# Kernel optimization log

Measured on AMD Instinct MI355X. Metric: run time of the kernel, lower is better.

Reference implementation:

```python
import jax, jax.numpy as jnp
import numpy as np

NS = 100000   # s-nodes (dtype==1, destinations)
NE = 100000   # e-nodes (dtype==2, sources)
EDG = 1600000 # edges e->s, avg degree 16
D = 256       # in_dim == out_dim
H = 8         # heads
HD = D // H   # head dim 32
FEAT = 64     # dst 'feat' size (hardcoded dstfeat_fc input)
DFF = 512     # ffn inner hidden


def setup_inputs() -> dict:
    key = jax.random.key(0)
    ks = jax.random.split(key, 12)
    s = jax.random.normal(ks[0], (NS, D), jnp.float32)
    e = jax.random.normal(ks[1], (NE, D), jnp.float32)
    dst_feat = jax.random.normal(ks[2], (NS, FEAT), jnp.float32)
    edge_src = jax.random.randint(ks[3], (EDG,), 0, NE)
    # guarantee every s-node has >=1 in-edge (first NS edges hit each dst once)
    rnd_dst = jax.random.randint(ks[4], (EDG,), 0, NS)
    edge_dst = jnp.where(jnp.arange(EDG) < NS, jnp.arange(EDG) % NS, rnd_dst)
    fc_w = jax.random.normal(ks[5], (H, D, HD), jnp.float32) / np.sqrt(D)
    dstfeat_w = jax.random.normal(ks[6], (H, FEAT, HD), jnp.float32) / np.sqrt(FEAT)
    proj_w = jax.random.normal(ks[7], (2 * D, D), jnp.float32) / np.sqrt(2 * D)
    proj_b = jnp.zeros((D,), jnp.float32)
    ln_g = jnp.ones((D,), jnp.float32)
    ln_b = jnp.zeros((D,), jnp.float32)
    w1 = jax.random.normal(ks[8], (D, DFF), jnp.float32) / np.sqrt(D)
    b1 = jnp.zeros((DFF,), jnp.float32)
    w2 = jax.random.normal(ks[9], (DFF, D), jnp.float32) / np.sqrt(DFF)
    b2 = jnp.zeros((D,), jnp.float32)
    return dict(s=s, e=e, dst_feat=dst_feat, fc_w=fc_w, dstfeat_w=dstfeat_w,
                proj_w=proj_w, proj_b=proj_b, ln_g=ln_g, ln_b=ln_b,
                w1=w1, b1=b1, w2=w2, b2=b2,
                edge_src=edge_src, edge_dst=edge_dst)


def _segment_softmax(scores, seg, n):
    # scores: [E, H], seg: [E] dst ids
    smax = jax.ops.segment_max(scores, seg, num_segments=n)  # [n, H], -inf for empty
    smax = jnp.where(jnp.isfinite(smax), smax, 0.0)
    ex = jnp.exp(scores - smax[seg])
    denom = jax.ops.segment_sum(ex, seg, num_segments=n)
    denom = jnp.where(denom > 0, denom, 1.0)
    return ex / denom[seg]


def reference(s, e, dst_feat, fc_w, dstfeat_w, proj_w, proj_b,
              ln_g, ln_b, w1, b1, w2, b2, edge_src, edge_dst):
    # per-head linear on source (e-node) features: [NE, H, HD]
    z = jnp.einsum('ni,hio->nho', e, fc_w)
    # per-head dst feature projection: [NS, H, HD]
    df = jnp.einsum('nf,hfo->nho', dst_feat, dstfeat_w)
    zs = z[edge_src]       # [E, H, HD] gather
    dfe = df[edge_dst]     # [E, H, HD]
    score = jnp.sum(zs * dfe, axis=-1)          # [E, H] per-edge dot score
    alpha = _segment_softmax(score, edge_dst, NS)
    hh = jax.ops.segment_sum(alpha[..., None] * zs, edge_dst, num_segments=NS)  # [NS, H, HD]
    h = hh.reshape(NS, H * HD)                  # concat heads
    h = jax.nn.elu(h)
    h = jnp.concatenate([h, s], axis=-1) @ proj_w + proj_b  # proj(cat(h, origin=s))
    # PositionwiseFeedForward (pre-LN, residual, gelu); dropout off (eval)
    mu = jnp.mean(h, axis=-1, keepdims=True)
    var = jnp.var(h, axis=-1, keepdims=True)
    xn = (h - mu) * jax.lax.rsqrt(var + 1e-6) * ln_g + ln_b
    out = h + (jax.nn.gelu(xn @ w1 + b1) @ w2 + b2)
    return out
```

## Files before the change

### kernel.cpp

```cpp
#include <hip/hip_runtime.h>
#include <hip/hip_bf16.h>
#include <stdint.h>

#define NS_N 100000
#define NE_N 100000
#define MP 100096
#define EDG_N 1600000
#define DIM 256
#define FEAT_N 64
#define DFF_N 512

using bf16 = __hip_bfloat16;
typedef __bf16 bf16x8 __attribute__((ext_vector_type(8)));
typedef float f32x4 __attribute__((ext_vector_type(4)));

__device__ __forceinline__ float toF(float x) { return x; }
__device__ __forceinline__ float toF(bf16 x) { return __bfloat162float(x); }

template <class T> __device__ __forceinline__ T fromF(float x);
template <> __device__ __forceinline__ float fromF<float>(float x) { return x; }
template <> __device__ __forceinline__ bf16 fromF<bf16>(float x) { return __float2bfloat16(x); }

__device__ __forceinline__ void g2l16(const void* g, void* l) {
    __builtin_amdgcn_global_load_lds((const __attribute__((address_space(1))) unsigned int*)g,
                                     (__attribute__((address_space(3))) unsigned int*)l, 16, 0, 0);
}

__global__ void cvt_f2b4(const float4* __restrict__ src, bf16* __restrict__ dst,
                         int M, int K4, int S) {
    int idx = blockIdx.x * 256 + threadIdx.x;
    if (idx >= M * K4) return;
    int r = idx / K4, c = (idx - r * K4) * 4;
    float4 v = src[idx];
    union { ushort4 u; bf16 h[4]; } p;
    p.h[0] = fromF<bf16>(v.x); p.h[1] = fromF<bf16>(v.y);
    p.h[2] = fromF<bf16>(v.z); p.h[3] = fromF<bf16>(v.w);
    *(ushort4*)&dst[(size_t)r * S + c] = p.u;
}

__global__ void tr_w(const float* __restrict__ src, bf16* __restrict__ dst, int K, int N) {
    int idx = blockIdx.x * 256 + threadIdx.x;
    if (idx >= K * N) return;
    int n = idx / K, k = idx - n * K;
    dst[idx] = fromF<bf16>(src[(size_t)k * N + n]);
}

__global__ void tr_headw(const float* __restrict__ src, bf16* __restrict__ dst, int K) {
    int idx = blockIdx.x * 256 + threadIdx.x;
    if (idx >= 256 * K) return;
    int n = idx / K, k = idx - n * K;
    dst[idx] = fromF<bf16>(src[((size_t)(n >> 5) * K + k) * 32 + (n & 31)]);
}

__global__ void count_edges(const int* __restrict__ edst, int* __restrict__ counts) {
    int t = blockIdx.x * 256 + threadIdx.x;
    if (t < EDG_N) atomicAdd(&counts[edst[t]], 1);
}

__global__ void scan_block(const int* __restrict__ counts, int* __restrict__ partial,
                           int* __restrict__ chunk) {
    __shared__ int sh[512];
    int i = blockIdx.x * 512 + threadIdx.x;
    int v = (i < NS_N) ? counts[i] : 0;
    sh[threadIdx.x] = v;
    __syncthreads();
    for (int off = 1; off < 512; off <<= 1) {
        int x = (threadIdx.x >= off) ? sh[threadIdx.x - off] : 0;
        __syncthreads();
        sh[threadIdx.x] += x;
        __syncthreads();
    }
    if (i < NS_N) partial[i] = sh[threadIdx.x] - v;
    if (threadIdx.x == 511) chunk[blockIdx.x] = sh[511];
}

__global__ void scan_chunks(int* __restrict__ chunk, int nc) {
    __shared__ int sh[256];
    int t = threadIdx.x;
    int v = (t < nc) ? chunk[t] : 0;
    sh[t] = v;
    __syncthreads();
    for (int off = 1; off < 256; off <<= 1) {
        int x = (t >= off) ? sh[t - off] : 0;
        __syncthreads();
        sh[t] += x;
        __syncthreads();
    }
    if (t < nc) chunk[t] = sh[t] - v;
}

__global__ void add_offsets(int* __restrict__ rowst, const int* __restrict__ chunk,
                            int* __restrict__ cursor) {
    int i = blockIdx.x * 256 + threadIdx.x;
    if (i < NS_N) {
        int r = rowst[i] + chunk[i >> 9];
        rowst[i] = r;
        cursor[i] = r;
    }
}

__global__ void scatter_edges(const int* __restrict__ esrc, const int* __restrict__ edst,
                              int* __restrict__ cursor, int* __restrict__ csr) {
    int t = blockIdx.x * 256 + threadIdx.x;
    if (t < EDG_N) {
        int d = edst[t];
        int pos = atomicAdd(&cursor[d], 1);
        csr[pos] = esrc[t];
    }
}

template <class TC, bool BIAS, bool GELU, bool RES>
__global__ __launch_bounds__(256) void mfma_gemm(
    const bf16* __restrict__ A, const bf16* __restrict__ BT,
    const float* __restrict__ bias, const float* __restrict__ res,
    TC* __restrict__ C, int M, int N, int K) {
    __shared__ bf16 As[128 * 32];
    __shared__ bf16 Bs[128 * 32];
    const int tid = threadIdx.x;
    const int wave = tid >> 6, lane = tid & 63;
    const int m0 = blockIdx.y * 128, n0 = blockIdx.x * 128;
    const int wm = (wave >> 1) * 64, wn = (wave & 1) * 64;

    f32x4 acc[4][4];
    const f32x4 zero4 = {0.f, 0.f, 0.f, 0.f};
#pragma unroll
    for (int i = 0; i < 4; i++)
#pragma unroll
        for (int j = 0; j < 4; j++) acc[i][j] = zero4;

    const int sr = lane >> 2, sc = (lane & 3) * 8;
    const bf16* gA0 = A + (size_t)(m0 + wave * 16 + sr) * K + sc;
    const bf16* gA1 = A + (size_t)(m0 + 64 + wave * 16 + sr) * K + sc;
    const bf16* gB0 = BT + (size_t)(n0 + wave * 16 + sr) * K + sc;
    const bf16* gB1 = BT + (size_t)(n0 + 64 + wave * 16 + sr) * K + sc;
    bf16* lA0 = As + wave * 512;
    bf16* lA1 = As + (wave + 4) * 512;
    bf16* lB0 = Bs + wave * 512;
    bf16* lB1 = Bs + (wave + 4) * 512;

    const int fr = lane & 15, fq = (lane >> 4) * 8;

    for (int k0 = 0; k0 < K; k0 += 32) {
        __syncthreads();
        g2l16(gA0, lA0);
        g2l16(gA1, lA1);
        g2l16(gB0, lB0);
        g2l16(gB1, lB1);
        gA0 += 32; gA1 += 32; gB0 += 32; gB1 += 32;
        __syncthreads();
        bf16x8 af[4], bfv[4];
#pragma unroll
        for (int mt = 0; mt < 4; mt++)
            af[mt] = *(const bf16x8*)&As[(wm + mt * 16 + fr) * 32 + fq];
#pragma unroll
        for (int nt = 0; nt < 4; nt++)
            bfv[nt] = *(const bf16x8*)&Bs[(wn + nt * 16 + fr) * 32 + fq];
#pragma unroll
        for (int mt = 0; mt < 4; mt++)
#pragma unroll
            for (int nt = 0; nt < 4; nt++)
                acc[mt][nt] = __builtin_amdgcn_mfma_f32_16x16x32_bf16(af[mt], bfv[nt], acc[mt][nt], 0, 0, 0);
    }

    const int q4 = (lane >> 4) * 4;
#pragma unroll
    for (int nt = 0; nt < 4; nt++) {
        const int col = n0 + wn + nt * 16 + fr;
        const float bv = BIAS ? bias[col] : 0.f;
#pragma unroll
        for (int mt = 0; mt < 4; mt++) {
#pragma unroll
            for (int r = 0; r < 4; r++) {
                int row = m0 + wm + mt * 16 + q4 + r;
                if (row < M) {
                    float v = acc[mt][nt][r] + bv;
                    if (GELU) {
                        float x = v;
                        v = 0.5f * x * (1.f + tanhf(0.7978845608028654f * (x + 0.044715f * x * x * x)));
                    }
                    if (RES) v += res[(size_t)row * N + col];
                    C[(size_t)row * N + col] = fromF<TC>(v);
                }
            }
        }
    }
}

__device__ __forceinline__ float4 ldz4(const bf16* __restrict__ p) {
    ushort4 u = *(const ushort4*)p;
    float4 f;
    f.x = toF(*(const bf16*)&u.x);
    f.y = toF(*(const bf16*)&u.y);
    f.z = toF(*(const bf16*)&u.z);
    f.w = toF(*(const bf16*)&u.w);
    return f;
}

__device__ __forceinline__ float dot4(float4 a, float4 b) {
    return fmaf(a.x, b.x, fmaf(a.y, b.y, fmaf(a.z, b.z, a.w * b.w)));
}

__device__ __forceinline__ float hred8(float p) {
    p += __shfl_xor(p, 1);
    p += __shfl_xor(p, 2);
    p += __shfl_xor(p, 4);
    return p;
}

__global__ __launch_bounds__(256) void attn_k(
    const bf16* __restrict__ z, const bf16* __restrict__ df,
    const int* __restrict__ rowst, const int* __restrict__ counts,
    const int* __restrict__ csr, bf16* __restrict__ he) {
    const int dst = blockIdx.x * 4 + (threadIdx.x >> 6);
    if (dst >= NS_N) return;
    const int lane = threadIdx.x & 63;
    const int c4 = lane * 4;

    float4 dfv = ldz4(&df[(size_t)dst * DIM + c4]);

    const int rs = rowst[dst], deg = counts[dst];
    float m = -1e30f, l = 0.f;
    float4 acc = {0.f, 0.f, 0.f, 0.f};

    for (int c0 = 0; c0 < deg; c0 += 64) {
        const int nc = min(64, deg - c0);
        int idx = (lane < nc) ? csr[rs + c0 + lane] : 0;
        int j = 0;
        for (; j + 4 <= nc; j += 4) {
            int s0 = __shfl(idx, j);
            int s1 = __shfl(idx, j + 1);
            int s2 = __shfl(idx, j + 2);
            int s3 = __shfl(idx, j + 3);
            float4 z0 = ldz4(&z[(size_t)s0 * DIM + c4]);
            float4 z1 = ldz4(&z[(size_t)s1 * DIM + c4]);
            float4 z2 = ldz4(&z[(size_t)s2 * DIM + c4]);
            float4 z3 = ldz4(&z[(size_t)s3 * DIM + c4]);
            float p0 = hred8(dot4(z0, dfv));
            float p1 = hred8(dot4(z1, dfv));
            float p2 = hred8(dot4(z2, dfv));
            float p3 = hred8(dot4(z3, dfv));
            float nm = fmaxf(m, fmaxf(fmaxf(p0, p1), fmaxf(p2, p3)));
            float e0 = __expf(m - nm);
            float w0 = __expf(p0 - nm);
            float w1 = __expf(p1 - nm);
            float w2 = __expf(p2 - nm);
            float w3 = __expf(p3 - nm);
            l = fmaf(l, e0, (w0 + w1) + (w2 + w3));
            acc.x = fmaf(acc.x, e0, fmaf(w0, z0.x, fmaf(w1, z1.x, fmaf(w2, z2.x, w3 * z3.x))));
            acc.y = fmaf(acc.y, e0, fmaf(w0, z0.y, fmaf(w1, z1.y, fmaf(w2, z2.y, w3 * z3.y))));
            acc.z = fmaf(acc.z, e0, fmaf(w0, z0.z, fmaf(w1, z1.z, fmaf(w2, z2.z, w3 * z3.z))));
            acc.w = fmaf(acc.w, e0, fmaf(w0, z0.w, fmaf(w1, z1.w, fmaf(w2, z2.w, w3 * z3.w))));
            m = nm;
        }
        for (; j < nc; ++j) {
            int s0 = __shfl(idx, j);
            float4 z0 = ldz4(&z[(size_t)s0 * DIM + c4]);
            float p0 = hred8(dot4(z0, dfv));
            float nm = fmaxf(m, p0);
            float e0 = __expf(m - nm);
            float w0 = __expf(p0 - nm);
            l = fmaf(l, e0, w0);
            acc.x = fmaf(acc.x, e0, w0 * z0.x);
            acc.y = fmaf(acc.y, e0, w0 * z0.y);
            acc.z = fmaf(acc.z, e0, w0 * z0.z);
            acc.w = fmaf(acc.w, e0, w0 * z0.w);
            m = nm;
        }
    }

    const float invl = 1.f / l;
    float hx = acc.x * invl, hy = acc.y * invl, hz = acc.z * invl, hw = acc.w * invl;
    hx = (hx > 0.f) ? hx : expm1f(hx);
    hy = (hy > 0.f) ? hy : expm1f(hy);
    hz = (hz > 0.f) ? hz : expm1f(hz);
    hw = (hw > 0.f) ? hw : expm1f(hw);
    union { ushort4 u; bf16 h[4]; } o;
    o.h[0] = fromF<bf16>(hx);
    o.h[1] = fromF<bf16>(hy);
    o.h[2] = fromF<bf16>(hz);
    o.h[3] = fromF<bf16>(hw);
    *(ushort4*)&he[(size_t)dst * 512 + c4] = o.u;
}

__global__ __launch_bounds__(256) void ln_k(const float* __restrict__ h1,
                                            const float* __restrict__ g,
                                            const float* __restrict__ b,
                                            bf16* __restrict__ xn) {
    int row = blockIdx.x, t = threadIdx.x;
    float x = h1[(size_t)row * DIM + t];
    float s1 = x, s2 = x * x;
#pragma unroll
    for (int off = 32; off > 0; off >>= 1) {
        s1 += __shfl_xor(s1, off, 64);
        s2 += __shfl_xor(s2, off, 64);
    }
    __shared__ float red[2][4];
    int w = t >> 6;
    if ((t & 63) == 0) {
        red[0][w] = s1;
        red[1][w] = s2;
    }
    __syncthreads();
    float t1 = red[0][0] + red[0][1] + red[0][2] + red[0][3];
    float t2 = red[1][0] + red[1][1] + red[1][2] + red[1][3];
    float mu = t1 * (1.f / DIM);
    float var = t2 * (1.f / DIM) - mu * mu;
    float v = (x - mu) * rsqrtf(var + 1e-6f) * g[t] + b[t];
    xn[(size_t)row * DIM + t] = fromF<bf16>(v);
}

extern "C" void kernel_launch(void* const* d_in, const int* in_sizes, int n_in,
                              void* d_out, int out_size, void* d_ws, size_t ws_size,
                              hipStream_t stream) {
    const float* s = (const float*)d_in[0];
    const float* e = (const float*)d_in[1];
    const float* dst_feat = (const float*)d_in[2];
    const float* fc_w = (const float*)d_in[3];
    const float* dstfeat_w = (const float*)d_in[4];
    const float* proj_w = (const float*)d_in[5];
    const float* proj_b = (const float*)d_in[6];
    const float* ln_g = (const float*)d_in[7];
    const float* ln_b = (const float*)d_in[8];
    const float* w1 = (const float*)d_in[9];
    const float* b1 = (const float*)d_in[10];
    const float* w2 = (const float*)d_in[11];
    const float* b2 = (const float*)d_in[12];
    const int* edge_src = (const int*)d_in[13];
    const int* edge_dst = (const int*)d_in[14];
    float* out = (float*)d_out;

    char* base = (char*)d_ws;
    size_t off = 0;
    auto alloc = [&](size_t bytes) -> char* {
        char* p = base + off;
        off = (off + bytes + 255) & ~(size_t)255;
        return p;
    };
    bf16* fcT = (bf16*)alloc((size_t)256 * 256 * 2);
    bf16* dfeatT = (bf16*)alloc((size_t)256 * 64 * 2);
    bf16* projT = (bf16*)alloc((size_t)256 * 512 * 2);
    bf16* w1T = (bf16*)alloc((size_t)512 * 256 * 2);
    bf16* w2T = (bf16*)alloc((size_t)256 * 512 * 2);
    int* counts = (int*)alloc((size_t)NS_N * 4);
    int* rowst = (int*)alloc((size_t)NS_N * 4);
    int* cursor = (int*)alloc((size_t)NS_N * 4);
    int* chunks = (int*)alloc(1024);
    int* csr = (int*)alloc((size_t)EDG_N * 4);
    bf16* eB = (bf16*)alloc((size_t)MP * DIM * 2);
    bf16* zB = (bf16*)alloc((size_t)MP * DIM * 2);
    bf16* dfB = (bf16*)alloc((size_t)MP * DIM * 2);
    bf16* dfeatB = (bf16*)alloc((size_t)MP * FEAT_N * 2);
    bf16* catB = (bf16*)alloc((size_t)MP * 512 * 2);
    float* h1F = (float*)alloc((size_t)MP * DIM * 4);
    bf16* xnB = eB;
    bf16* a1B = zB;

    hipMemsetAsync(counts, 0, (size_t)NS_N * 4, stream);
    tr_headw<<<(256 * 256 + 255) / 256, 256, 0, stream>>>(fc_w, fcT, 256);
    tr_headw<<<(256 * 64 + 255) / 256, 256, 0, stream>>>(dstfeat_w, dfeatT, 64);
    tr_w<<<(512 * 256 + 255) / 256, 256, 0, stream>>>(proj_w, projT, 512, 256);
    tr_w<<<(256 * 512 + 255) / 256, 256, 0, stream>>>(w1, w1T, 256, 512);
    tr_w<<<(512 * 256 + 255) / 256, 256, 0, stream>>>(w2, w2T, 512, 256);
    cvt_f2b4<<<(NE_N * 64 + 255) / 256, 256, 0, stream>>>((const float4*)e, eB, NE_N, 64, DIM);
    cvt_f2b4<<<(NS_N * 16 + 255) / 256, 256, 0, stream>>>((const float4*)dst_feat, dfeatB, NS_N, 16, FEAT_N);
    cvt_f2b4<<<(NS_N * 64 + 255) / 256, 256, 0, stream>>>((const float4*)s, catB + 256, NS_N, 64, 512);
    count_edges<<<(EDG_N + 255) / 256, 256, 0, stream>>>(edge_dst, counts);
    int nchunk = (NS_N + 511) / 512;
    scan_block<<<nchunk, 512, 0, stream>>>(counts, rowst, chunks);
    scan_chunks<<<1, 256, 0, stream>>>(chunks, nchunk);
    add_offsets<<<(NS_N + 255) / 256, 256, 0, stream>>>(rowst, chunks, cursor);
    scatter_edges<<<(EDG_N + 255) / 256, 256, 0, stream>>>(edge_src, edge_dst, cursor, csr);

    dim3 blk(256);
    const int gy = MP / 128;
    mfma_gemm<bf16, false, false, false><<<dim3(2, gy), blk, 0, stream>>>(
        eB, fcT, nullptr, nullptr, zB, NE_N, DIM, DIM);
    mfma_gemm<bf16, false, false, false><<<dim3(2, gy), blk, 0, stream>>>(
        dfeatB, dfeatT, nullptr, nullptr, dfB, NS_N, DIM, FEAT_N);
    attn_k<<<(NS_N + 3) / 4, 256, 0, stream>>>(zB, dfB, rowst, counts, csr, catB);
    mfma_gemm<float, true, false, false><<<dim3(2, gy), blk, 0, stream>>>(
        catB, projT, proj_b, nullptr, h1F, NS_N, DIM, 2 * DIM);
    ln_k<<<NS_N, 256, 0, stream>>>(h1F, ln_g, ln_b, xnB);
    mfma_gemm<bf16, true, true, false><<<dim3(4, gy), blk, 0, stream>>>(
        xnB, w1T, b1, nullptr, a1B, NS_N, DFF_N, DIM);
    mfma_gemm<float, true, false, true><<<dim3(2, gy), blk, 0, stream>>>(
        a1B, w2T, b2, h1F, out, NS_N, DIM, DFF_N);
}
```

Measured before the change: 1.088 ms.

## Triple-buffer GEMM LDS tiles with async prefetch and XOR-swizzled layout

The MFMA GEMM now keeps three LDS buffers and issues global-to-LDS loads two k-tiles ahead. It waits with explicit vmcnt counts instead of a full sync before each tile, so memory latency overlaps the MFMA work. It also XOR-swizzles the column placement of each 16-byte chunk, both when loading global data into LDS and when reading fragments, to cut LDS bank conflicts. LDS use triples, which may lower occupancy. The hand-written waitcnt counts assume a fixed number of outstanding loads per stage.

```diff
diff --git a/kernel.cpp b/kernel.cpp
--- a/kernel.cpp
+++ b/kernel.cpp
@@ -114,8 +114,8 @@
     const bf16* __restrict__ A, const bf16* __restrict__ BT,
     const float* __restrict__ bias, const float* __restrict__ res,
     TC* __restrict__ C, int M, int N, int K) {
-    __shared__ bf16 As[128 * 32];
-    __shared__ bf16 Bs[128 * 32];
+    __shared__ bf16 As[3][128 * 32];
+    __shared__ bf16 Bs[3][128 * 32];
     const int tid = threadIdx.x;
     const int wave = tid >> 6, lane = tid & 63;
     const int m0 = blockIdx.y * 128, n0 = blockIdx.x * 128;
@@ -128,44 +128,60 @@
 #pragma unroll
         for (int j = 0; j < 4; j++) acc[i][j] = zero4;
 
-    const int sr = lane >> 2, sc = (lane & 3) * 8;
-    const bf16* gA0 = A + (size_t)(m0 + wave * 16 + sr) * K + sc;
-    const bf16* gA1 = A + (size_t)(m0 + 64 + wave * 16 + sr) * K + sc;
-    const bf16* gB0 = BT + (size_t)(n0 + wave * 16 + sr) * K + sc;
-    const bf16* gB1 = BT + (size_t)(n0 + 64 + wave * 16 + sr) * K + sc;
-    bf16* lA0 = As + wave * 512;
-    bf16* lA1 = As + (wave + 4) * 512;
-    bf16* lB0 = Bs + wave * 512;
-    bf16* lB1 = Bs + (wave + 4) * 512;
-
-    const int fr = lane & 15, fq = (lane >> 4) * 8;
-
-    for (int k0 = 0; k0 < K; k0 += 32) {
-        __syncthreads();
-        g2l16(gA0, lA0);
-        g2l16(gA1, lA1);
-        g2l16(gB0, lB0);
-        g2l16(gB1, lB1);
-        gA0 += 32; gA1 += 32; gB0 += 32; gB1 += 32;
-        __syncthreads();
+    const int sr = lane >> 2;
+    const int scs = (((lane & 3) ^ ((lane >> 3) & 3)) * 8);
+    const bf16* gA0 = A + (size_t)(m0 + wave * 16 + sr) * K + scs;
+    const bf16* gA1 = A + (size_t)(m0 + 64 + wave * 16 + sr) * K + scs;
+    const bf16* gB0 = BT + (size_t)(n0 + wave * 16 + sr) * K + scs;
+    const bf16* gB1 = BT + (size_t)(n0 + 64 + wave * 16 + sr) * K + scs;
+
+    const int nt = K >> 5;
+
+    auto stage = [&](int kt, int b) {
+        const int ko = kt << 5;
+        g2l16(gA0 + ko, &As[b][wave * 512]);
+        g2l16(gA1 + ko, &As[b][(wave + 4) * 512]);
+        g2l16(gB0 + ko, &Bs[b][wave * 512]);
+        g2l16(gB1 + ko, &Bs[b][(wave + 4) * 512]);
+    };
+
+    stage(0, 0);
+    if (nt > 1) stage(1, 1);
+
+    const int fr = lane & 15;
+    const int pslot = ((((lane >> 4) ^ ((fr >> 1) & 3))) << 4);
+
+    int buf = 0;
+    for (int t = 0; t < nt; ++t) {
+        if (t + 2 < nt) stage(t + 2, buf == 0 ? 2 : buf - 1);
+        if (t + 2 < nt)      asm volatile("s_waitcnt vmcnt(8)" ::: "memory");
+        else if (t + 1 < nt) asm volatile("s_waitcnt vmcnt(4)" ::: "memory");
+        else                 asm volatile("s_waitcnt vmcnt(0)" ::: "memory");
+        __builtin_amdgcn_s_barrier();
+        asm volatile("" ::: "memory");
+        const char* Ab = (const char*)As[buf];
+        const char* Bb = (const char*)Bs[buf];
         bf16x8 af[4], bfv[4];
 #pragma unroll
         for (int mt = 0; mt < 4; mt++)
-            af[mt] = *(const bf16x8*)&As[(wm + mt * 16 + fr) * 32 + fq];
-#pragma unroll
-        for (int nt = 0; nt < 4; nt++)
-            bfv[nt] = *(const bf16x8*)&Bs[(wn + nt * 16 + fr) * 32 + fq];
+            af[mt] = *(const bf16x8*)(Ab + (wm + mt * 16 + fr) * 64 + pslot);
+#pragma unroll
+        for (int jt = 0; jt < 4; jt++)
+            bfv[jt] = *(const bf16x8*)(Bb + (wn + jt * 16 + fr) * 64 + pslot);
 #pragma unroll
         for (int mt = 0; mt < 4; mt++)
 #pragma unroll
-            for (int nt = 0; nt < 4; nt++)
-                acc[mt][nt] = __builtin_amdgcn_mfma_f32_16x16x32_bf16(af[mt], bfv[nt], acc[mt][nt], 0, 0, 0);
+            for (int jt = 0; jt < 4; jt++)
+                acc[mt][jt] = __builtin_amdgcn_mfma_f32_16x16x32_bf16(af[mt], bfv[jt], acc[mt][jt], 0, 0, 0);
+        asm volatile("" ::: "memory");
+        __builtin_amdgcn_s_barrier();
+        buf = (buf == 2) ? 0 : buf + 1;
     }
 
     const int q4 = (lane >> 4) * 4;
 #pragma unroll
-    for (int nt = 0; nt < 4; nt++) {
-        const int col = n0 + wn + nt * 16 + fr;
+    for (int jt = 0; jt < 4; jt++) {
+        const int col = n0 + wn + jt * 16 + fr;
         const float bv = BIAS ? bias[col] : 0.f;
 #pragma unroll
         for (int mt = 0; mt < 4; mt++) {
@@ -173,7 +189,7 @@
             for (int r = 0; r < 4; r++) {
                 int row = m0 + wm + mt * 16 + q4 + r;
                 if (row < M) {
-                    float v = acc[mt][nt][r] + bv;
+                    float v = acc[mt][jt][r] + bv;
                     if (GELU) {
                         float x = v;
                         v = 0.5f * x * (1.f + tanhf(0.7978845608028654f * (x + 0.044715f * x * x * x)));
```

Result: no change. 1.069 ms (-1.7%).

## Rewrite GEMMs as full-K A-stationary tiles with B streamed from global

Applied to the files above, without the earlier changes.

Replaces the 128x128 K-looped GEMM with a kernel that loads a whole 64xK A panel into swizzled LDS once. Each wave then sweeps output column blocks, streaming B fragments directly from global memory (L2-resident weights) with register double buffering. The aim is to drop per-K-step barriers and the redundant A reloads across column blocks. It also folds bias and residual into the accumulator init and swaps tanhf for an exp-based tanh in GELU. LDS use grows to 64 KB for K=512, which may limit occupancy, and global B loads may add latency.

```diff
diff --git a/kernel.cpp b/kernel.cpp
--- a/kernel.cpp
+++ b/kernel.cpp
@@ -109,77 +109,100 @@
     }
 }
 
-template <class TC, bool BIAS, bool GELU, bool RES>
-__global__ __launch_bounds__(256) void mfma_gemm(
+template <int K, int N, class TC, bool BIAS, bool GELU, bool RES>
+__global__ __launch_bounds__(256) void mfma_gemm2(
     const bf16* __restrict__ A, const bf16* __restrict__ BT,
     const float* __restrict__ bias, const float* __restrict__ res,
-    TC* __restrict__ C, int M, int N, int K) {
-    __shared__ bf16 As[128 * 32];
-    __shared__ bf16 Bs[128 * 32];
+    TC* __restrict__ C, int M) {
+    static_assert(K % 32 == 0 && N % 256 == 0, "shape");
+    constexpr int KS = K / 32;
+    constexpr int CHUNKS = K / 32;
+    __shared__ bf16 As[64 * K];
+
     const int tid = threadIdx.x;
     const int wave = tid >> 6, lane = tid & 63;
-    const int m0 = blockIdx.y * 128, n0 = blockIdx.x * 128;
-    const int wm = (wave >> 1) * 64, wn = (wave & 1) * 64;
-
-    f32x4 acc[4][4];
-    const f32x4 zero4 = {0.f, 0.f, 0.f, 0.f};
-#pragma unroll
-    for (int i = 0; i < 4; i++)
-#pragma unroll
-        for (int j = 0; j < 4; j++) acc[i][j] = zero4;
-
-    const int sr = lane >> 2, sc = (lane & 3) * 8;
-    const bf16* gA0 = A + (size_t)(m0 + wave * 16 + sr) * K + sc;
-    const bf16* gA1 = A + (size_t)(m0 + 64 + wave * 16 + sr) * K + sc;
-    const bf16* gB0 = BT + (size_t)(n0 + wave * 16 + sr) * K + sc;
-    const bf16* gB1 = BT + (size_t)(n0 + 64 + wave * 16 + sr) * K + sc;
-    bf16* lA0 = As + wave * 512;
-    bf16* lA1 = As + (wave + 4) * 512;
-    bf16* lB0 = Bs + wave * 512;
-    bf16* lB1 = Bs + (wave + 4) * 512;
-
-    const int fr = lane & 15, fq = (lane >> 4) * 8;
-
-    for (int k0 = 0; k0 < K; k0 += 32) {
-        __syncthreads();
-        g2l16(gA0, lA0);
-        g2l16(gA1, lA1);
-        g2l16(gB0, lB0);
-        g2l16(gB1, lB1);
-        gA0 += 32; gA1 += 32; gB0 += 32; gB1 += 32;
-        __syncthreads();
-        bf16x8 af[4], bfv[4];
-#pragma unroll
-        for (int mt = 0; mt < 4; mt++)
-            af[mt] = *(const bf16x8*)&As[(wm + mt * 16 + fr) * 32 + fq];
-#pragma unroll
-        for (int nt = 0; nt < 4; nt++)
-            bfv[nt] = *(const bf16x8*)&Bs[(wn + nt * 16 + fr) * 32 + fq];
-#pragma unroll
-        for (int mt = 0; mt < 4; mt++)
-#pragma unroll
-            for (int nt = 0; nt < 4; nt++)
-                acc[mt][nt] = __builtin_amdgcn_mfma_f32_16x16x32_bf16(af[mt], bfv[nt], acc[mt][nt], 0, 0, 0);
-    }
-
-    const int q4 = (lane >> 4) * 4;
-#pragma unroll
-    for (int nt = 0; nt < 4; nt++) {
-        const int col = n0 + wn + nt * 16 + fr;
-        const float bv = BIAS ? bias[col] : 0.f;
-#pragma unroll
-        for (int mt = 0; mt < 4; mt++) {
-#pragma unroll
-            for (int r = 0; r < 4; r++) {
-                int row = m0 + wm + mt * 16 + q4 + r;
-                if (row < M) {
-                    float v = acc[mt][nt][r] + bv;
-                    if (GELU) {
-                        float x = v;
-                        v = 0.5f * x * (1.f + tanhf(0.7978845608028654f * (x + 0.044715f * x * x * x)));
+    const int m0 = blockIdx.x * 64;
+
+#pragma unroll
+    for (int c = 0; c < CHUNKS; ++c) {
+        int off = c * 1024 + lane * 16;
+        int riw = off / (K * 2);
+        int slot = (off % (K * 2)) / 16;
+        int row = wave * 16 + riw;
+        const bf16* g = A + (size_t)(m0 + row) * K + (slot ^ (row & 7)) * 8;
+        g2l16(g, As + (size_t)wave * 16 * K + c * 512);
+    }
+    __syncthreads();
+
+    const int fr = lane & 15, q = lane >> 4;
+    const int f7 = fr & 7;
+    const int q4 = q * 4;
+
+    for (int nc = wave * 64; nc < N; nc += 256) {
+        f32x4 acc[4][4];
+#pragma unroll
+        for (int jt = 0; jt < 4; jt++) {
+            const int col = nc + jt * 16 + fr;
+            const float bv = BIAS ? bias[col] : 0.f;
+#pragma unroll
+            for (int mt = 0; mt < 4; mt++) {
+#pragma unroll
+                for (int r = 0; r < 4; r++) {
+                    float v = bv;
+                    if (RES) v += res[(size_t)(m0 + mt * 16 + q4 + r) * N + col];
+                    acc[mt][jt][r] = v;
+                }
+            }
+        }
+
+        bf16x8 bcur[4];
+#pragma unroll
+        for (int jt = 0; jt < 4; jt++)
+            bcur[jt] = *(const bf16x8*)(BT + (size_t)(nc + jt * 16 + fr) * K + q * 8);
+#pragma unroll
+        for (int ks = 0; ks < KS; ++ks) {
+            bf16x8 bnxt[4];
+            if (ks + 1 < KS) {
+#pragma unroll
+                for (int jt = 0; jt < 4; jt++)
+                    bnxt[jt] = *(const bf16x8*)(BT + (size_t)(nc + jt * 16 + fr) * K + (ks + 1) * 32 + q * 8);
+            }
+            const int slot = (ks * 4 + q) ^ f7;
+            bf16x8 af[4];
+#pragma unroll
+            for (int mt = 0; mt < 4; mt++)
+                af[mt] = *(const bf16x8*)(As + (size_t)(mt * 16 + fr) * K + slot * 8);
+#pragma unroll
+            for (int mt = 0; mt < 4; mt++)
+#pragma unroll
+                for (int jt = 0; jt < 4; jt++)
+                    acc[mt][jt] = __builtin_amdgcn_mfma_f32_16x16x32_bf16(af[mt], bcur[jt], acc[mt][jt], 0, 0, 0);
+            if (ks + 1 < KS) {
+#pragma unroll
+                for (int jt = 0; jt < 4; jt++) bcur[jt] = bnxt[jt];
+            }
+        }
+
+#pragma unroll
+        for (int jt = 0; jt < 4; jt++) {
+            const int col = nc + jt * 16 + fr;
+#pragma unroll
+            for (int mt = 0; mt < 4; mt++) {
+#pragma unroll
+                for (int r = 0; r < 4; r++) {
+                    const int row = m0 + mt * 16 + q4 + r;
+                    if (row < M) {
+                        float v = acc[mt][jt][r];
+                        if (GELU) {
+                            float x = v;
+                            float u = 0.7978845608028654f * (x + 0.044715f * x * x * x);
+                            float eu = __expf(-2.f * fabsf(u));
+                            float th = (1.f - eu) / (1.f + eu);
+                            th = (u >= 0.f) ? th : -th;
+                            v = 0.5f * x * (1.f + th);
+                        }
+                        C[(size_t)row * N + col] = fromF<TC>(v);
                     }
-                    if (RES) v += res[(size_t)row * N + col];
-                    C[(size_t)row * N + col] = fromF<TC>(v);
                 }
             }
         }
@@ -372,17 +395,17 @@
     scatter_edges<<<(EDG_N + 255) / 256, 256, 0, stream>>>(edge_src, edge_dst, cursor, csr);
 
     dim3 blk(256);
-    const int gy = MP / 128;
-    mfma_gemm<bf16, false, false, false><<<dim3(2, gy), blk, 0, stream>>>(
-        eB, fcT, nullptr, nullptr, zB, NE_N, DIM, DIM);
-    mfma_gemm<bf16, false, false, false><<<dim3(2, gy), blk, 0, stream>>>(
-        dfeatB, dfeatT, nullptr, nullptr, dfB, NS_N, DIM, FEAT_N);
+    const int gb = MP / 64;
+    mfma_gemm2<256, 256, bf16, false, false, false><<<gb, blk, 0, stream>>>(
+        eB, fcT, nullptr, nullptr, zB, NE_N);
+    mfma_gemm2<64, 256, bf16, false, false, false><<<gb, blk, 0, stream>>>(
+        dfeatB, dfeatT, nullptr, nullptr, dfB, NS_N);
     attn_k<<<(NS_N + 3) / 4, 256, 0, stream>>>(zB, dfB, rowst, counts, csr, catB);
-    mfma_gemm<float, true, false, false><<<dim3(2, gy), blk, 0, stream>>>(
-        catB, projT, proj_b, nullptr, h1F, NS_N, DIM, 2 * DIM);
+    mfma_gemm2<512, 256, float, true, false, false><<<gb, blk, 0, stream>>>(
+        catB, projT, proj_b, nullptr, h1F, NS_N);
     ln_k<<<NS_N, 256, 0, stream>>>(h1F, ln_g, ln_b, xnB);
-    mfma_gemm<bf16, true, true, false><<<dim3(4, gy), blk, 0, stream>>>(
-        xnB, w1T, b1, nullptr, a1B, NS_N, DFF_N, DIM);
-    mfma_gemm<float, true, false, true><<<dim3(2, gy), blk, 0, stream>>>(
-        a1B, w2T, b2, h1F, out, NS_N, DIM, DFF_N);
-}
+    mfma_gemm2<256, 512, bf16, true, true, false><<<gb, blk, 0, stream>>>(
+        xnB, w1T, b1, nullptr, a1B, NS_N);
+    mfma_gemm2<512, 256, float, true, false, true><<<gb, blk, 0, stream>>>(
+        a1B, w2T, b2, h1F, out, NS_N);
+}
```

Result: no change. 1.097 ms (+0.8%).
